# Kernel tuning notes

Measured on AMD Instinct MI355X. Metric: run time of the kernel, lower is better.

The kernel has to match this reference:

```python
import jax, jax.numpy as jnp
import numpy as np

N = 100000
E = 3200000
HEADS = 4
DH = 16  # per-head dim
IN = 300
OUT2 = 32
SLOPE = 0.2  # PyG GATConv leaky_relu negative slope


def setup_inputs() -> dict:
    key = jax.random.key(0)
    ks = jax.random.split(key, 10)
    x = jax.random.normal(ks[0], (N, IN), dtype=jnp.float32)
    edge_index = jax.random.randint(ks[1], (2, E), 0, N, dtype=jnp.int64)
    sec_order_edge_index = jax.random.randint(ks[2], (2, E), 0, N, dtype=jnp.int64)
    # GATConv(300, 16, heads=4) params
    W1 = jax.random.normal(ks[3], (IN, HEADS * DH), dtype=jnp.float32) * (1.0 / np.sqrt(IN))
    att_src = jax.random.normal(ks[4], (HEADS, DH), dtype=jnp.float32) * 0.1
    att_dst = jax.random.normal(ks[5], (HEADS, DH), dtype=jnp.float32) * 0.1
    b1 = jnp.zeros((HEADS * DH,), dtype=jnp.float32)
    # GCNConv(64, 32) params
    W2 = jax.random.normal(ks[6], (HEADS * DH, OUT2), dtype=jnp.float32) * (1.0 / np.sqrt(HEADS * DH))
    b2 = jnp.zeros((OUT2,), dtype=jnp.float32)
    return {"x": x, "W1": W1, "att_src": att_src, "att_dst": att_dst, "b1": b1,
            "W2": W2, "b2": b2, "edge_index": edge_index,
            "sec_order_edge_index": sec_order_edge_index}


def _add_self_loops(edge_index, n):
    loop = jnp.arange(n, dtype=edge_index.dtype)
    src = jnp.concatenate([edge_index[0], loop])
    dst = jnp.concatenate([edge_index[1], loop])
    return src, dst


def _gat(x, W1, att_src, att_dst, b1, edge_index):
    n = x.shape[0]
    src, dst = _add_self_loops(edge_index, n)
    h = (x @ W1).reshape(n, HEADS, DH)                    # [N,H,D]
    a_s = jnp.einsum('nhd,hd->nh', h, att_src)            # [N,H]
    a_d = jnp.einsum('nhd,hd->nh', h, att_dst)
    e = jax.nn.leaky_relu(a_s[src] + a_d[dst], SLOPE)     # [Et,H]
    # segment softmax over edges grouped by destination node
    m = jax.ops.segment_max(e, dst, num_segments=n)       # [N,H]
    ex = jnp.exp(e - m[dst])
    denom = jax.ops.segment_sum(ex, dst, num_segments=n)  # [N,H] (>0: self-loops)
    alpha = ex / denom[dst]                               # [Et,H]
    out = jax.ops.segment_sum(h[src] * alpha[:, :, None], dst, num_segments=n)
    return out.reshape(n, HEADS * DH) + b1


def _gcn(x, W2, b2, edge_index):
    n = x.shape[0]
    src, dst = _add_self_loops(edge_index, n)
    deg = jax.ops.segment_sum(jnp.ones_like(dst, dtype=x.dtype), dst, num_segments=n)
    dinv = jnp.where(deg > 0, jax.lax.rsqrt(deg), 0.0)
    norm = dinv[src] * dinv[dst]                          # [Et]
    h = x @ W2                                            # [N,32]
    out = jax.ops.segment_sum(h[src] * norm[:, None], dst, num_segments=n)
    return out + b2


def reference(x, W1, att_src, att_dst, b1, W2, b2, edge_index, sec_order_edge_index):
    x1 = jax.nn.relu(_gat(x, W1, att_src, att_dst, b1, edge_index))
    # F.dropout with training=False is identity (eval mode)
    return _gcn(x1, W2, b2, sec_order_edge_index)
```

## Files before the change

kernel.cpp:

```cpp
#include <hip/hip_runtime.h>
#include <hip/hip_fp16.h>

#define N_NODES 100000
#define N_EDGES 3200000
#define TOT_E   (N_EDGES + N_NODES)
#define HEADS   4
#define DH      16
#define IN_F    300
#define HID     64
#define OUT2    32
#define SLOPE   0.2f
#define NBK     256
#define GSZ     391
#define EBLK    4096
#define NBA     ((TOT_E + EBLK - 1) / EBLK)

typedef _Float16 f16x8 __attribute__((ext_vector_type(8)));
typedef float    f32x4 __attribute__((ext_vector_type(4)));

__global__ void k_wcvt(const float* __restrict__ W1, __half* __restrict__ BT16) {
    int idx = blockIdx.x * 256 + threadIdx.x;
    if (idx >= HID * 320) return;
    int n = idx / 320, k = idx - n * 320;
    BT16[idx] = (k < IN_F) ? __float2half(W1[(size_t)k * HID + n]) : __float2half(0.f);
}

#define G1_BM 128
#define G1_BK 64
#define G1_NS 5

__global__ __launch_bounds__(256) void k_gemm1(const float* __restrict__ x,
                                               const __half* __restrict__ BT16,
                                               __half* __restrict__ h16) {
    __shared__ _Float16 At[G1_BM][G1_BK];
    __shared__ _Float16 Bt[HID][G1_BK];
    const int t = threadIdx.x;
    const int lane = t & 63, w = t >> 6;
    const int lr = lane & 15, lg = lane >> 4;
    const int row0 = blockIdx.x * G1_BM;
    const int wrow = w * 32;

    int arow[4], auc[4];
    const float* axp[4];
#pragma unroll
    for (int m = 0; m < 4; m++) {
        int id = t + m * 256;
        arow[m] = id >> 3; auc[m] = id & 7;
        int gr = row0 + arow[m];
        gr = (gr < N_NODES) ? gr : (N_NODES - 1);
        axp[m] = x + (size_t)gr * IN_F + auc[m] * 8;
    }
    int bn[2], buc[2];
    const __half* bxp[2];
#pragma unroll
    for (int q = 0; q < 2; q++) {
        int id = t + q * 256;
        bn[q] = id >> 3; buc[q] = id & 7;
        bxp[q] = BT16 + bn[q] * (G1_BK * G1_NS) + buc[q] * 8;
    }

    float4 ar[4][2];
    uint4  br[2];

    auto loadS = [&](int kb) {
        if (kb + G1_BK <= IN_F) {
#pragma unroll
            for (int m = 0; m < 4; m++) {
                ar[m][0] = *(const float4*)(axp[m] + kb);
                ar[m][1] = *(const float4*)(axp[m] + kb + 4);
            }
        } else {
#pragma unroll
            for (int m = 0; m < 4; m++) {
                float v[8];
#pragma unroll
                for (int e = 0; e < 8; e++) {
                    int k = kb + auc[m] * 8 + e;
                    v[e] = (k < IN_F) ? axp[m][kb + e] : 0.f;
                }
                ar[m][0] = make_float4(v[0], v[1], v[2], v[3]);
                ar[m][1] = make_float4(v[4], v[5], v[6], v[7]);
            }
        }
#pragma unroll
        for (int q = 0; q < 2; q++) br[q] = *(const uint4*)(bxp[q] + kb);
    };

    auto writeS = [&]() {
#pragma unroll
        for (int m = 0; m < 4; m++) {
            f16x8 pk;
            pk[0] = (_Float16)ar[m][0].x; pk[1] = (_Float16)ar[m][0].y;
            pk[2] = (_Float16)ar[m][0].z; pk[3] = (_Float16)ar[m][0].w;
            pk[4] = (_Float16)ar[m][1].x; pk[5] = (_Float16)ar[m][1].y;
            pk[6] = (_Float16)ar[m][1].z; pk[7] = (_Float16)ar[m][1].w;
            *(f16x8*)&At[arow[m]][(auc[m] ^ (arow[m] & 7)) << 3] = pk;
        }
#pragma unroll
        for (int q = 0; q < 2; q++)
            *(uint4*)&Bt[bn[q]][(buc[q] ^ (bn[q] & 7)) << 3] = br[q];
    };

    f32x4 acc[2][4];
#pragma unroll
    for (int mt = 0; mt < 2; mt++)
#pragma unroll
        for (int nt = 0; nt < 4; nt++) acc[mt][nt] = (f32x4){0.f, 0.f, 0.f, 0.f};

    loadS(0);
    for (int s = 0; s < G1_NS; s++) {
        __syncthreads();
        writeS();
        if (s + 1 < G1_NS) loadS((s + 1) * G1_BK);
        __syncthreads();
#pragma unroll
        for (int ks = 0; ks < 2; ks++) {
            const int u = ks * 4 + lg;
            f16x8 af[2], bf[4];
#pragma unroll
            for (int mt = 0; mt < 2; mt++) {
                int r = wrow + mt * 16 + lr;
                af[mt] = *(const f16x8*)&At[r][(u ^ (r & 7)) << 3];
            }
#pragma unroll
            for (int nt = 0; nt < 4; nt++) {
                int n = nt * 16 + lr;
                bf[nt] = *(const f16x8*)&Bt[n][(u ^ (n & 7)) << 3];
            }
#pragma unroll
            for (int mt = 0; mt < 2; mt++)
#pragma unroll
                for (int nt = 0; nt < 4; nt++)
                    acc[mt][nt] = __builtin_amdgcn_mfma_f32_16x16x32_f16(
                        af[mt], bf[nt], acc[mt][nt], 0, 0, 0);
        }
    }

#pragma unroll
    for (int mt = 0; mt < 2; mt++) {
#pragma unroll
        for (int rg = 0; rg < 4; rg++) {
            int gr = row0 + wrow + mt * 16 + lg * 4 + rg;
            if (gr < N_NODES) {
#pragma unroll
                for (int nt = 0; nt < 4; nt++)
                    h16[(size_t)gr * HID + nt * 16 + lr] =
                        __float2half((float)acc[mt][nt][rg]);
            }
        }
    }
}

__global__ void k_scores(const __half* __restrict__ h16,
                         const float* __restrict__ att_src,
                         const float* __restrict__ att_dst,
                         float* __restrict__ as_ad) {
    int tid = blockIdx.x * blockDim.x + threadIdx.x;
    if (tid >= N_NODES * HEADS) return;
    int n = tid >> 2, hd = tid & 3;
    const __half* hp = &h16[(size_t)n * HID + hd * DH];
    __half2 hv[8];
    *(float4*)&hv[0] = *(const float4*)hp;
    *(float4*)&hv[4] = *(const float4*)(hp + 8);
    float s = 0.f, d = 0.f;
#pragma unroll
    for (int k = 0; k < 8; k++) {
        float2 f = __half22float2(hv[k]);
        s += f.x * att_src[hd * DH + 2 * k] + f.y * att_src[hd * DH + 2 * k + 1];
        d += f.x * att_dst[hd * DH + 2 * k] + f.y * att_dst[hd * DH + 2 * k + 1];
    }
    as_ad[n * 8 + hd] = s;
    as_ad[n * 8 + 4 + hd] = d;
}

__global__ __launch_bounds__(512) void k_chist(const int* __restrict__ ei1,
                                               const int* __restrict__ ei2,
                                               int* __restrict__ ccnt) {
    __shared__ int hist[NBK];
    int b = blockIdx.x; const int* ei; int* cc;
    if (b < NBA) { ei = ei1; cc = ccnt; }
    else         { ei = ei2; cc = ccnt + NBK; b -= NBA; }
    int t = threadIdx.x;
    if (t < NBK) hist[t] = 0;
    __syncthreads();
    int e0 = b * EBLK;
#pragma unroll
    for (int i = 0; i < 8; i++) {
        int e = e0 + i * 512 + t;
        if (e < TOT_E) {
            int dst = (e < N_EDGES) ? ei[N_EDGES + e] : (e - N_EDGES);
            atomicAdd(&hist[(unsigned int)dst / GSZ], 1);
        }
    }
    __syncthreads();
    if (t < NBK) { int v = hist[t]; if (v) atomicAdd(&cc[t], v); }
}

__global__ __launch_bounds__(512) void k_cscan(const int* __restrict__ ccnt,
                                               int* __restrict__ crp,
                                               int* __restrict__ ccur) {
    __shared__ int sc[512];
    int t = threadIdx.x;
    int idx = t & (NBK - 1);
    int own = ccnt[t];
    sc[t] = own;
    __syncthreads();
    for (int off = 1; off < NBK; off <<= 1) {
        int v = (idx >= off) ? sc[t - off] : 0;
        __syncthreads();
        sc[t] += v;
        __syncthreads();
    }
    int ex = sc[t] - own;
    crp[t] = ex; ccur[t] = ex;
}

__global__ __launch_bounds__(512) void k_binA(const int* __restrict__ ei1,
                                              const int* __restrict__ ei2,
                                              int* __restrict__ ccur,
                                              unsigned int* __restrict__ tmp) {
    __shared__ int hist[NBK];
    __shared__ int base[NBK];
    int b = blockIdx.x; const int* ei; int loff;
    if (b < NBA) { ei = ei1; loff = 0; }
    else         { ei = ei2; loff = 1; b -= NBA; }
    int t = threadIdx.x;
    if (t < NBK) hist[t] = 0;
    __syncthreads();
    unsigned int pk[8]; int cb[8], rk[8];
    int e0 = b * EBLK;
#pragma unroll
    for (int i = 0; i < 8; i++) {
        int e = e0 + i * 512 + t;
        cb[i] = -1;
        if (e < TOT_E) {
            int src, dst;
            if (e < N_EDGES) { src = ei[e]; dst = ei[N_EDGES + e]; }
            else             { src = e - N_EDGES; dst = src; }
            unsigned int c   = (unsigned int)dst / GSZ;
            unsigned int dlo = (unsigned int)dst - c * GSZ;
            cb[i] = (int)c;
            pk[i] = (dlo << 17) | (unsigned int)src;
            rk[i] = atomicAdd(&hist[c], 1);
        }
    }
    __syncthreads();
    if (t < NBK) {
        int v = hist[t];
        base[t] = v ? atomicAdd(&ccur[loff * NBK + t], v) : 0;
    }
    __syncthreads();
    unsigned int* tp = tmp + (size_t)loff * TOT_E;
#pragma unroll
    for (int i = 0; i < 8; i++)
        if (cb[i] >= 0) tp[base[cb[i]] + rk[i]] = pk[i];
}

__global__ __launch_bounds__(256) void k_binB(const unsigned int* __restrict__ tmp,
                                              const int* __restrict__ crp,
                                              int* __restrict__ rowptr,
                                              int* __restrict__ srcs,
                                              float* __restrict__ dinv) {
    __shared__ int cnt[GSZ + 1];
    __shared__ int sc[512];
    __shared__ int cur[GSZ + 1];
    int blk = blockIdx.x;
    int l = blk >> 8, b = blk & 255;
    int t = threadIdx.x;
    int nbeg = b * GSZ;
    int ncnt = min(GSZ, N_NODES - nbeg);
    const int* crpl = crp + l * NBK;
    int ebeg = crpl[b];
    int eend = (b < NBK - 1) ? crpl[b + 1] : TOT_E;
    const unsigned int* tp = tmp + (size_t)l * TOT_E;
    for (int i = t; i < GSZ + 1; i += 256) cnt[i] = 0;
    __syncthreads();
    for (int e = ebeg + t; e < eend; e += 256)
        atomicAdd(&cnt[tp[e] >> 17], 1);
    __syncthreads();
    int t2 = t + 256;
    sc[t]  = (t  < ncnt) ? cnt[t]  : 0;
    sc[t2] = (t2 < ncnt) ? cnt[t2] : 0;
    __syncthreads();
    for (int off = 1; off < 512; off <<= 1) {
        int v0 = (t  >= off) ? sc[t  - off] : 0;
        int v1 = (t2 >= off) ? sc[t2 - off] : 0;
        __syncthreads();
        sc[t] += v0; sc[t2] += v1;
        __syncthreads();
    }
    for (int i = t; i < ncnt; i += 256) {
        int c = cnt[i];
        int gpos = ebeg + sc[i] - c;
        rowptr[l * N_NODES + nbeg + i] = gpos;
        cur[i] = gpos;
        if (l == 1) dinv[nbeg + i] = rsqrtf((float)c);
    }
    __syncthreads();
    int* so = srcs + (size_t)l * TOT_E;
    for (int e = ebeg + t; e < eend; e += 256) {
        unsigned int p = tp[e];
        int pos = atomicAdd(&cur[p >> 17], 1);
        so[pos] = (int)(p & 0x1FFFF);
    }
}

__global__ __launch_bounds__(256) void k_gat(const __half* __restrict__ h16,
                                             const float* __restrict__ as_ad,
                                             const int* __restrict__ rowptr,
                                             const int* __restrict__ srcs,
                                             const float* __restrict__ b1,
                                             float* __restrict__ x1) {
    int w = (blockIdx.x * 256 + threadIdx.x) >> 6;
    if (w >= N_NODES) return;
    int lane = threadIdx.x & 63;
    int eidx = lane >> 3;
    int cl = lane & 7;
    int hd = cl >> 1;
    int c0 = cl * 8;
    float ad = as_ad[w * 8 + 4 + hd];
    int beg = rowptr[w];
    int end = (w == N_NODES - 1) ? TOT_E : rowptr[w + 1];
    float l = 0.f;
    float a0 = 0.f, a1 = 0.f, a2 = 0.f, a3 = 0.f;
    float a4 = 0.f, a5 = 0.f, a6 = 0.f, a7 = 0.f;
#pragma unroll 2
    for (int j = beg; j < end; j += 8) {
        int je = j + eidx;
        int s = srcs[min(je, end - 1)];
        float4 raw = *(const float4*)&h16[(size_t)s * HID + c0];
        float e = as_ad[s * 8 + hd] + ad;
        e = fminf(fmaxf(e, SLOPE * e), 60.f);
        float p = (je < end) ? __expf(e) : 0.f;
        l += p;
        const __half2* hv = (const __half2*)&raw;
        float2 f0 = __half22float2(hv[0]);
        float2 f1 = __half22float2(hv[1]);
        float2 f2 = __half22float2(hv[2]);
        float2 f3 = __half22float2(hv[3]);
        a0 += p * f0.x; a1 += p * f0.y; a2 += p * f1.x; a3 += p * f1.y;
        a4 += p * f2.x; a5 += p * f2.y; a6 += p * f3.x; a7 += p * f3.y;
    }
    l  += __shfl_xor(l, 8, 64);  l  += __shfl_xor(l, 16, 64);  l  += __shfl_xor(l, 32, 64);
    a0 += __shfl_xor(a0, 8, 64); a0 += __shfl_xor(a0, 16, 64); a0 += __shfl_xor(a0, 32, 64);
    a1 += __shfl_xor(a1, 8, 64); a1 += __shfl_xor(a1, 16, 64); a1 += __shfl_xor(a1, 32, 64);
    a2 += __shfl_xor(a2, 8, 64); a2 += __shfl_xor(a2, 16, 64); a2 += __shfl_xor(a2, 32, 64);
    a3 += __shfl_xor(a3, 8, 64); a3 += __shfl_xor(a3, 16, 64); a3 += __shfl_xor(a3, 32, 64);
    a4 += __shfl_xor(a4, 8, 64); a4 += __shfl_xor(a4, 16, 64); a4 += __shfl_xor(a4, 32, 64);
    a5 += __shfl_xor(a5, 8, 64); a5 += __shfl_xor(a5, 16, 64); a5 += __shfl_xor(a5, 32, 64);
    a6 += __shfl_xor(a6, 8, 64); a6 += __shfl_xor(a6, 16, 64); a6 += __shfl_xor(a6, 32, 64);
    a7 += __shfl_xor(a7, 8, 64); a7 += __shfl_xor(a7, 16, 64); a7 += __shfl_xor(a7, 32, 64);
    if (eidx == 0) {
        float rl = 1.f / l;
        float4 b0 = *(const float4*)&b1[c0];
        float4 b4 = *(const float4*)&b1[c0 + 4];
        float4 o0 = make_float4(fmaxf(a0 * rl + b0.x, 0.f),
                                fmaxf(a1 * rl + b0.y, 0.f),
                                fmaxf(a2 * rl + b0.z, 0.f),
                                fmaxf(a3 * rl + b0.w, 0.f));
        float4 o4 = make_float4(fmaxf(a4 * rl + b4.x, 0.f),
                                fmaxf(a5 * rl + b4.y, 0.f),
                                fmaxf(a6 * rl + b4.z, 0.f),
                                fmaxf(a7 * rl + b4.w, 0.f));
        *(float4*)&x1[(size_t)w * HID + c0] = o0;
        *(float4*)&x1[(size_t)w * HID + c0 + 4] = o4;
    }
}

__global__ __launch_bounds__(256) void k_gemm2(const float* __restrict__ x1,
                                               const float* __restrict__ W2,
                                               const float* __restrict__ dinv,
                                               __half* __restrict__ h2s) {
    __shared__ float wl[HID * OUT2];
    __shared__ float xl[8][HID];
    int t = threadIdx.x;
    for (int i = t; i < HID * OUT2; i += 256) wl[i] = W2[i];
    int row0 = blockIdx.x * 8;
    for (int i = t; i < 8 * HID; i += 256) {
        int rr = i >> 6, kk = i & 63;
        int gr = row0 + rr;
        xl[rr][kk] = (gr < N_NODES) ? x1[(size_t)gr * HID + kk] : 0.f;
    }
    __syncthreads();
    int r = t >> 5, c = t & 31;
    float acc = 0.f;
#pragma unroll 8
    for (int k = 0; k < HID; k++) acc += xl[r][k] * wl[k * OUT2 + c];
    int gr = row0 + r;
    if (gr < N_NODES) h2s[(size_t)gr * OUT2 + c] = __float2half(acc * dinv[gr]);
}

__global__ __launch_bounds__(256) void k_gcn(const __half* __restrict__ h2s,
                                             const float* __restrict__ dinv,
                                             const int* __restrict__ rowptr,
                                             const int* __restrict__ srcs,
                                             const float* __restrict__ b2,
                                             float* __restrict__ out) {
    int w = (blockIdx.x * 256 + threadIdx.x) >> 6;
    if (w >= N_NODES) return;
    int lane = threadIdx.x & 63;
    int eidx = lane >> 2;
    int cq = lane & 3;
    int c0 = cq * 8;
    int beg = rowptr[w];
    int end = (w == N_NODES - 1) ? TOT_E : rowptr[w + 1];
    float a0 = 0.f, a1 = 0.f, a2 = 0.f, a3 = 0.f;
    float a4 = 0.f, a5 = 0.f, a6 = 0.f, a7 = 0.f;
#pragma unroll 2
    for (int j = beg; j < end; j += 16) {
        int je = j + eidx;
        int s = srcs[min(je, end - 1)];
        uint4 raw = *(const uint4*)&h2s[(size_t)s * OUT2 + c0];
        if (je < end) {
            const __half2* hv = (const __half2*)&raw;
            float2 f0 = __half22float2(hv[0]);
            float2 f1 = __half22float2(hv[1]);
            float2 f2 = __half22float2(hv[2]);
            float2 f3 = __half22float2(hv[3]);
            a0 += f0.x; a1 += f0.y; a2 += f1.x; a3 += f1.y;
            a4 += f2.x; a5 += f2.y; a6 += f3.x; a7 += f3.y;
        }
    }
    a0 += __shfl_xor(a0, 4, 64); a0 += __shfl_xor(a0, 8, 64); a0 += __shfl_xor(a0, 16, 64); a0 += __shfl_xor(a0, 32, 64);
    a1 += __shfl_xor(a1, 4, 64); a1 += __shfl_xor(a1, 8, 64); a1 += __shfl_xor(a1, 16, 64); a1 += __shfl_xor(a1, 32, 64);
    a2 += __shfl_xor(a2, 4, 64); a2 += __shfl_xor(a2, 8, 64); a2 += __shfl_xor(a2, 16, 64); a2 += __shfl_xor(a2, 32, 64);
    a3 += __shfl_xor(a3, 4, 64); a3 += __shfl_xor(a3, 8, 64); a3 += __shfl_xor(a3, 16, 64); a3 += __shfl_xor(a3, 32, 64);
    a4 += __shfl_xor(a4, 4, 64); a4 += __shfl_xor(a4, 8, 64); a4 += __shfl_xor(a4, 16, 64); a4 += __shfl_xor(a4, 32, 64);
    a5 += __shfl_xor(a5, 4, 64); a5 += __shfl_xor(a5, 8, 64); a5 += __shfl_xor(a5, 16, 64); a5 += __shfl_xor(a5, 32, 64);
    a6 += __shfl_xor(a6, 4, 64); a6 += __shfl_xor(a6, 8, 64); a6 += __shfl_xor(a6, 16, 64); a6 += __shfl_xor(a6, 32, 64);
    a7 += __shfl_xor(a7, 4, 64); a7 += __shfl_xor(a7, 8, 64); a7 += __shfl_xor(a7, 16, 64); a7 += __shfl_xor(a7, 32, 64);
    if (eidx == 0) {
        float dv = dinv[w];
        float4 b0 = *(const float4*)&b2[c0];
        float4 b4 = *(const float4*)&b2[c0 + 4];
        float4 o0 = make_float4(a0 * dv + b0.x, a1 * dv + b0.y,
                                a2 * dv + b0.z, a3 * dv + b0.w);
        float4 o4 = make_float4(a4 * dv + b4.x, a5 * dv + b4.y,
                                a6 * dv + b4.z, a7 * dv + b4.w);
        *(float4*)&out[(size_t)w * OUT2 + c0] = o0;
        *(float4*)&out[(size_t)w * OUT2 + c0 + 4] = o4;
    }
}

static inline size_t align_up(size_t v, size_t a) { return (v + a - 1) & ~(a - 1); }

extern "C" void kernel_launch(void* const* d_in, const int* in_sizes, int n_in,
                              void* d_out, int out_size, void* d_ws, size_t ws_size,
                              hipStream_t stream) {
    const float* x       = (const float*)d_in[0];
    const float* W1      = (const float*)d_in[1];
    const float* att_src = (const float*)d_in[2];
    const float* att_dst = (const float*)d_in[3];
    const float* b1      = (const float*)d_in[4];
    const float* W2      = (const float*)d_in[5];
    const float* b2      = (const float*)d_in[6];
    const int*   ei1     = (const int*)d_in[7];
    const int*   ei2     = (const int*)d_in[8];
    float* out = (float*)d_out;

    char* p = (char*)d_ws;
    size_t off = 0;
    auto carve = [&](size_t bytes) { void* q = p + off; off = align_up(off + bytes, 256); return q; };
    __half* h16   = (__half*)carve((size_t)N_NODES * HID * 2);
    float* x1     = (float*)carve((size_t)N_NODES * HID * 4);
    __half* h2s   = (__half*)carve((size_t)N_NODES * OUT2 * 2);
    float* as_ad  = (float*)carve((size_t)N_NODES * 8 * 4);
    float* dinv   = (float*)carve((size_t)N_NODES * 4);
    int* rowptr   = (int*)carve((size_t)2 * N_NODES * 4);
    int* srcs     = (int*)carve((size_t)2 * TOT_E * 4);
    int* ccnt     = (int*)carve((size_t)2 * NBK * 4);
    int* crp      = (int*)carve((size_t)2 * NBK * 4);
    int* ccur     = (int*)carve((size_t)2 * NBK * 4);
    __half* BT16  = (__half*)carve((size_t)HID * 320 * 2);
    unsigned int* tmp = (unsigned int*)x1;
    (void)ws_size; (void)in_sizes; (void)n_in; (void)out_size;

    hipMemsetAsync(ccnt, 0, (size_t)2 * NBK * 4, stream);

    k_wcvt<<<(HID * 320 + 255) / 256, 256, 0, stream>>>(W1, BT16);
    k_gemm1<<<(N_NODES + G1_BM - 1) / G1_BM, 256, 0, stream>>>(x, BT16, h16);
    k_scores<<<(N_NODES * HEADS + 255) / 256, 256, 0, stream>>>(h16, att_src, att_dst, as_ad);

    k_chist<<<2 * NBA, 512, 0, stream>>>(ei1, ei2, ccnt);
    k_cscan<<<1, 512, 0, stream>>>(ccnt, crp, ccur);
    k_binA<<<2 * NBA, 512, 0, stream>>>(ei1, ei2, ccur, tmp);
    k_binB<<<2 * NBK, 256, 0, stream>>>(tmp, crp, rowptr, srcs, dinv);

    k_gat<<<N_NODES / 4, 256, 0, stream>>>(h16, as_ad, rowptr, srcs, b1, x1);

    k_gemm2<<<N_NODES / 8, 256, 0, stream>>>(x1, W2, dinv, h2s);

    k_gcn<<<N_NODES / 4, 256, 0, stream>>>(h2s, dinv, rowptr + N_NODES, srcs + TOT_E, b2, out);
}
```

Baseline: 553.9 us.

## Fuse attention scores into GEMM1, store GAT output as fp16, retile GEMM2

The per-node attention score computation moves into the GEMM1 epilogue using lane shuffles, so the separate k_scores kernel and its reread of h16 go away. The GAT output x1 is now written as fp16, halving that intermediate's traffic, and GEMM2 handles 32 rows per block with 4 accumulators per thread. Source-index loads use nontemporal hints, and the binning temp buffer gets its own allocation instead of aliasing x1. In exchange there is extra fp16 rounding of the hidden activations and a larger workspace.

```diff
diff --git a/kernel.cpp b/kernel.cpp
--- a/kernel.cpp
+++ b/kernel.cpp
@@ -31,7 +31,10 @@
 
 __global__ __launch_bounds__(256) void k_gemm1(const float* __restrict__ x,
                                                const __half* __restrict__ BT16,
-                                               __half* __restrict__ h16) {
+                                               const float* __restrict__ att_src,
+                                               const float* __restrict__ att_dst,
+                                               __half* __restrict__ h16,
+                                               float* __restrict__ as_ad) {
     __shared__ _Float16 At[G1_BM][G1_BK];
     __shared__ _Float16 Bt[HID][G1_BK];
     const int t = threadIdx.x;
@@ -136,41 +139,43 @@
         }
     }
 
+    float ws4[4], wd4[4];
+#pragma unroll
+    for (int nt = 0; nt < 4; nt++) {
+        ws4[nt] = att_src[nt * DH + lr];
+        wd4[nt] = att_dst[nt * DH + lr];
+    }
+
 #pragma unroll
     for (int mt = 0; mt < 2; mt++) {
 #pragma unroll
         for (int rg = 0; rg < 4; rg++) {
             int gr = row0 + wrow + mt * 16 + lg * 4 + rg;
+            float s_[4], d_[4];
+#pragma unroll
+            for (int nt = 0; nt < 4; nt++) {
+                float v = (float)acc[mt][nt][rg];
+                float vs = v * ws4[nt], vd = v * wd4[nt];
+                vs += __shfl_xor(vs, 1, 64); vs += __shfl_xor(vs, 2, 64);
+                vs += __shfl_xor(vs, 4, 64); vs += __shfl_xor(vs, 8, 64);
+                vd += __shfl_xor(vd, 1, 64); vd += __shfl_xor(vd, 2, 64);
+                vd += __shfl_xor(vd, 4, 64); vd += __shfl_xor(vd, 8, 64);
+                s_[nt] = vs; d_[nt] = vd;
+            }
             if (gr < N_NODES) {
 #pragma unroll
                 for (int nt = 0; nt < 4; nt++)
                     h16[(size_t)gr * HID + nt * 16 + lr] =
                         __float2half((float)acc[mt][nt][rg]);
+                if (lr == 0) {
+                    *(float4*)&as_ad[gr * 8] =
+                        make_float4(s_[0], s_[1], s_[2], s_[3]);
+                    *(float4*)&as_ad[gr * 8 + 4] =
+                        make_float4(d_[0], d_[1], d_[2], d_[3]);
+                }
             }
         }
     }
-}
-
-__global__ void k_scores(const __half* __restrict__ h16,
-                         const float* __restrict__ att_src,
-                         const float* __restrict__ att_dst,
-                         float* __restrict__ as_ad) {
-    int tid = blockIdx.x * blockDim.x + threadIdx.x;
-    if (tid >= N_NODES * HEADS) return;
-    int n = tid >> 2, hd = tid & 3;
-    const __half* hp = &h16[(size_t)n * HID + hd * DH];
-    __half2 hv[8];
-    *(float4*)&hv[0] = *(const float4*)hp;
-    *(float4*)&hv[4] = *(const float4*)(hp + 8);
-    float s = 0.f, d = 0.f;
-#pragma unroll
-    for (int k = 0; k < 8; k++) {
-        float2 f = __half22float2(hv[k]);
-        s += f.x * att_src[hd * DH + 2 * k] + f.y * att_src[hd * DH + 2 * k + 1];
-        d += f.x * att_dst[hd * DH + 2 * k] + f.y * att_dst[hd * DH + 2 * k + 1];
-    }
-    as_ad[n * 8 + hd] = s;
-    as_ad[n * 8 + 4 + hd] = d;
 }
 
 __global__ __launch_bounds__(512) void k_chist(const int* __restrict__ ei1,
@@ -310,7 +315,7 @@
                                              const int* __restrict__ rowptr,
                                              const int* __restrict__ srcs,
                                              const float* __restrict__ b1,
-                                             float* __restrict__ x1) {
+                                             __half* __restrict__ x1h) {
     int w = (blockIdx.x * 256 + threadIdx.x) >> 6;
     if (w >= N_NODES) return;
     int lane = threadIdx.x & 63;
@@ -327,8 +332,8 @@
 #pragma unroll 2
     for (int j = beg; j < end; j += 8) {
         int je = j + eidx;
-        int s = srcs[min(je, end - 1)];
-        float4 raw = *(const float4*)&h16[(size_t)s * HID + c0];
+        int s = __builtin_nontemporal_load(&srcs[min(je, end - 1)]);
+        uint4 raw = *(const uint4*)&h16[(size_t)s * HID + c0];
         float e = as_ad[s * 8 + hd] + ad;
         e = fminf(fmaxf(e, SLOPE * e), 60.f);
         float p = (je < end) ? __expf(e) : 0.f;
@@ -354,40 +359,54 @@
         float rl = 1.f / l;
         float4 b0 = *(const float4*)&b1[c0];
         float4 b4 = *(const float4*)&b1[c0 + 4];
-        float4 o0 = make_float4(fmaxf(a0 * rl + b0.x, 0.f),
-                                fmaxf(a1 * rl + b0.y, 0.f),
-                                fmaxf(a2 * rl + b0.z, 0.f),
-                                fmaxf(a3 * rl + b0.w, 0.f));
-        float4 o4 = make_float4(fmaxf(a4 * rl + b4.x, 0.f),
-                                fmaxf(a5 * rl + b4.y, 0.f),
-                                fmaxf(a6 * rl + b4.z, 0.f),
-                                fmaxf(a7 * rl + b4.w, 0.f));
-        *(float4*)&x1[(size_t)w * HID + c0] = o0;
-        *(float4*)&x1[(size_t)w * HID + c0 + 4] = o4;
-    }
-}
-
-__global__ __launch_bounds__(256) void k_gemm2(const float* __restrict__ x1,
+        f16x8 o;
+        o[0] = (_Float16)fmaxf(a0 * rl + b0.x, 0.f);
+        o[1] = (_Float16)fmaxf(a1 * rl + b0.y, 0.f);
+        o[2] = (_Float16)fmaxf(a2 * rl + b0.z, 0.f);
+        o[3] = (_Float16)fmaxf(a3 * rl + b0.w, 0.f);
+        o[4] = (_Float16)fmaxf(a4 * rl + b4.x, 0.f);
+        o[5] = (_Float16)fmaxf(a5 * rl + b4.y, 0.f);
+        o[6] = (_Float16)fmaxf(a6 * rl + b4.z, 0.f);
+        o[7] = (_Float16)fmaxf(a7 * rl + b4.w, 0.f);
+        *(f16x8*)&x1h[(size_t)w * HID + c0] = o;
+    }
+}
+
+__global__ __launch_bounds__(256) void k_gemm2(const __half* __restrict__ x1h,
                                                const float* __restrict__ W2,
                                                const float* __restrict__ dinv,
                                                __half* __restrict__ h2s) {
     __shared__ float wl[HID * OUT2];
-    __shared__ float xl[8][HID];
+    __shared__ float xl[32][HID];
     int t = threadIdx.x;
     for (int i = t; i < HID * OUT2; i += 256) wl[i] = W2[i];
-    int row0 = blockIdx.x * 8;
-    for (int i = t; i < 8 * HID; i += 256) {
-        int rr = i >> 6, kk = i & 63;
-        int gr = row0 + rr;
-        xl[rr][kk] = (gr < N_NODES) ? x1[(size_t)gr * HID + kk] : 0.f;
-    }
-    __syncthreads();
-    int r = t >> 5, c = t & 31;
-    float acc = 0.f;
+    int row0 = blockIdx.x * 32;
+    {
+        int rr = t >> 3, kk0 = (t & 7) * 8;
+        uint4 raw = *(const uint4*)&x1h[(size_t)(row0 + rr) * HID + kk0];
+        const __half2* hv = (const __half2*)&raw;
+#pragma unroll
+        for (int q = 0; q < 4; q++) {
+            float2 f = __half22float2(hv[q]);
+            xl[rr][kk0 + 2 * q] = f.x;
+            xl[rr][kk0 + 2 * q + 1] = f.y;
+        }
+    }
+    __syncthreads();
+    int r0 = (t >> 5) * 4, c = t & 31;
+    float ac0 = 0.f, ac1 = 0.f, ac2 = 0.f, ac3 = 0.f;
 #pragma unroll 8
-    for (int k = 0; k < HID; k++) acc += xl[r][k] * wl[k * OUT2 + c];
-    int gr = row0 + r;
-    if (gr < N_NODES) h2s[(size_t)gr * OUT2 + c] = __float2half(acc * dinv[gr]);
+    for (int k = 0; k < HID; k++) {
+        float wv = wl[k * OUT2 + c];
+        ac0 += xl[r0 + 0][k] * wv;
+        ac1 += xl[r0 + 1][k] * wv;
+        ac2 += xl[r0 + 2][k] * wv;
+        ac3 += xl[r0 + 3][k] * wv;
+    }
+    h2s[(size_t)(row0 + r0 + 0) * OUT2 + c] = __float2half(ac0 * dinv[row0 + r0 + 0]);
+    h2s[(size_t)(row0 + r0 + 1) * OUT2 + c] = __float2half(ac1 * dinv[row0 + r0 + 1]);
+    h2s[(size_t)(row0 + r0 + 2) * OUT2 + c] = __float2half(ac2 * dinv[row0 + r0 + 2]);
+    h2s[(size_t)(row0 + r0 + 3) * OUT2 + c] = __float2half(ac3 * dinv[row0 + r0 + 3]);
 }
 
 __global__ __launch_bounds__(256) void k_gcn(const __half* __restrict__ h2s,
@@ -409,7 +428,7 @@
 #pragma unroll 2
     for (int j = beg; j < end; j += 16) {
         int je = j + eidx;
-        int s = srcs[min(je, end - 1)];
+        int s = __builtin_nontemporal_load(&srcs[min(je, end - 1)]);
         uint4 raw = *(const uint4*)&h2s[(size_t)s * OUT2 + c0];
         if (je < end) {
             const __half2* hv = (const __half2*)&raw;
@@ -462,33 +481,32 @@
     size_t off = 0;
     auto carve = [&](size_t bytes) { void* q = p + off; off = align_up(off + bytes, 256); return q; };
     __half* h16   = (__half*)carve((size_t)N_NODES * HID * 2);
-    float* x1     = (float*)carve((size_t)N_NODES * HID * 4);
+    __half* x1h   = (__half*)carve((size_t)N_NODES * HID * 2);
     __half* h2s   = (__half*)carve((size_t)N_NODES * OUT2 * 2);
     float* as_ad  = (float*)carve((size_t)N_NODES * 8 * 4);
     float* dinv   = (float*)carve((size_t)N_NODES * 4);
     int* rowptr   = (int*)carve((size_t)2 * N_NODES * 4);
     int* srcs     = (int*)carve((size_t)2 * TOT_E * 4);
+    unsigned int* tmp = (unsigned int*)carve((size_t)2 * TOT_E * 4);
     int* ccnt     = (int*)carve((size_t)2 * NBK * 4);
     int* crp      = (int*)carve((size_t)2 * NBK * 4);
     int* ccur     = (int*)carve((size_t)2 * NBK * 4);
     __half* BT16  = (__half*)carve((size_t)HID * 320 * 2);
-    unsigned int* tmp = (unsigned int*)x1;
     (void)ws_size; (void)in_sizes; (void)n_in; (void)out_size;
 
     hipMemsetAsync(ccnt, 0, (size_t)2 * NBK * 4, stream);
 
     k_wcvt<<<(HID * 320 + 255) / 256, 256, 0, stream>>>(W1, BT16);
-    k_gemm1<<<(N_NODES + G1_BM - 1) / G1_BM, 256, 0, stream>>>(x, BT16, h16);
-    k_scores<<<(N_NODES * HEADS + 255) / 256, 256, 0, stream>>>(h16, att_src, att_dst, as_ad);
+    k_gemm1<<<(N_NODES + G1_BM - 1) / G1_BM, 256, 0, stream>>>(x, BT16, att_src, att_dst, h16, as_ad);
 
     k_chist<<<2 * NBA, 512, 0, stream>>>(ei1, ei2, ccnt);
     k_cscan<<<1, 512, 0, stream>>>(ccnt, crp, ccur);
     k_binA<<<2 * NBA, 512, 0, stream>>>(ei1, ei2, ccur, tmp);
     k_binB<<<2 * NBK, 256, 0, stream>>>(tmp, crp, rowptr, srcs, dinv);
 
-    k_gat<<<N_NODES / 4, 256, 0, stream>>>(h16, as_ad, rowptr, srcs, b1, x1);
-
-    k_gemm2<<<N_NODES / 8, 256, 0, stream>>>(x1, W2, dinv, h2s);
+    k_gat<<<N_NODES / 4, 256, 0, stream>>>(h16, as_ad, rowptr, srcs, b1, x1h);
+
+    k_gemm2<<<N_NODES / 32, 256, 0, stream>>>(x1h, W2, dinv, h2s);
 
     k_gcn<<<N_NODES / 4, 256, 0, stream>>>(h2s, dinv, rowptr + N_NODES, srcs + TOT_E, b2, out);
 }
```

Result: no change. 549.0 us (-0.9%).
